# Kernel tuning notes

Hardware: AMD Instinct MI355X
Metric: run time of the kernel (lower is better)

Reference implementation:

```python
import jax, jax.numpy as jnp
import numpy as np

SEQ, BATCH, INPUT = 2048, 64, 16
HEADS, HID = 8, 64  # per-head hidden = hidden_size/output_size = 512/8


def setup_inputs() -> dict:
    key = jax.random.key(0)
    ks = jax.random.split(key, 8)
    s = 1.0 / np.sqrt(HID)  # PyTorch LSTM/Linear init scale
    return {
        "x": jax.random.normal(ks[0], (SEQ, BATCH, INPUT), jnp.float32),
        "W_ih": jax.random.uniform(ks[1], (HEADS, 4 * HID, INPUT), jnp.float32, -s, s),
        "W_hh": jax.random.uniform(ks[2], (HEADS, 4 * HID, HID), jnp.float32, -s, s),
        "b_ih": jax.random.uniform(ks[3], (HEADS, 4 * HID), jnp.float32, -s, s),
        "b_hh": jax.random.uniform(ks[4], (HEADS, 4 * HID), jnp.float32, -s, s),
        "W_lin": jax.random.uniform(ks[5], (HEADS, HID), jnp.float32, -s, s),
        "b_lin": jax.random.uniform(ks[6], (HEADS,), jnp.float32, -s, s),
    }


def _multihead_lstm(x, W_ih, W_hh, b_ih, b_hh):
    # x: (T,B,I); weights stacked over heads H. PyTorch gate order: i,f,g,o.
    T, B = x.shape[0], x.shape[1]
    H, G = W_hh.shape[0], W_hh.shape[1]  # G = 4*hid
    hid = G // 4
    # Input projection for all timesteps/heads at once: (T,B,H,4h)
    xp = jnp.einsum("tbi,hgi->tbhg", x, W_ih) + b_ih + b_hh

    def step(carry, xt):
        h_prev, c_prev = carry  # (B,H,hid)
        z = xt + jnp.einsum("bhk,hgk->bhg", h_prev, W_hh)  # (B,H,4h)
        i = jax.nn.sigmoid(z[..., 0 * hid:1 * hid])
        f = jax.nn.sigmoid(z[..., 1 * hid:2 * hid])
        g = jnp.tanh(z[..., 2 * hid:3 * hid])
        o = jax.nn.sigmoid(z[..., 3 * hid:4 * hid])
        c = f * c_prev + i * g
        h = o * jnp.tanh(c)
        return (h, c), h

    zeros = jnp.zeros((B, H, hid), x.dtype)
    _, hs = jax.lax.scan(step, (zeros, zeros), xp)  # hs: (T,B,H,hid)
    return hs


def reference(x, W_ih, W_hh, b_ih, b_hh, W_lin, b_lin):
    hs = _multihead_lstm(x, W_ih, W_hh, b_ih, b_hh)  # (T,B,H,hid)
    # per-head Linear(hid -> 1), concatenated over heads -> (T,B,H)
    out = jnp.einsum("tbhk,hk->tbh", hs, W_lin) + b_lin
    # lstm_output accumulates (sums) the per-head hidden trajectories
    lstm_output = hs.sum(axis=2)  # (T,B,hid)
    return out, lstm_output
```

## Files before the change

kernel.cpp:

```cpp
#include <hip/hip_runtime.h>
#include <hip/hip_fp16.h>

#define TT   2048
#define BB   64
#define II   16
#define HH   8
#define HIDN 64
#define GG   256
#define T4   (TT / 4)

typedef _Float16 h2 __attribute__((ext_vector_type(2)));
typedef _Float16 h4 __attribute__((ext_vector_type(4)));
typedef _Float16 h8 __attribute__((ext_vector_type(8)));

__device__ __forceinline__ float fdot2(h2 a, h2 b, float c) {
    return __builtin_amdgcn_fdot2(a, b, c, false);
}
__device__ __forceinline__ float fast_sigmoid(float z) {
    return __builtin_amdgcn_rcpf(1.0f + __expf(-z));
}
__device__ __forceinline__ float fast_tanh(float z) {
    return fmaf(2.0f, __builtin_amdgcn_rcpf(1.0f + __expf(-2.0f * z)), -1.0f);
}

__global__ void cvt_x_kernel(const float* __restrict__ x, _Float16* __restrict__ xh, int n4) {
    int i = blockIdx.x * blockDim.x + threadIdx.x;
    if (i < n4) {
        float4 v = ((const float4*)x)[i];
        ((h2*)xh)[2 * i]     = h2{ (_Float16)v.x, (_Float16)v.y };
        ((h2*)xh)[2 * i + 1] = h2{ (_Float16)v.z, (_Float16)v.w };
    }
}

template <int STAGE, bool XF16>
__global__ __launch_bounds__(64, 1)
void lstm_wave(const float* __restrict__ x,
               const _Float16* __restrict__ xh,
               const float* __restrict__ Wih,
               const float* __restrict__ Whh,
               const float* __restrict__ bih,
               const float* __restrict__ bhh,
               const float* __restrict__ Wlin,
               const float* __restrict__ blin,
               float* __restrict__ out,
               float* __restrict__ lstm_out,
               _Float16* __restrict__ stage_f16)
{
    const int lane = threadIdx.x;
    const int c    = blockIdx.x;
    const int b    = c & (BB - 1);
    const int hd   = c >> 6;

    h2 whh[4][HIDN / 2];
    h2 wih[4][II / 2];
    float bias[4];
#pragma unroll
    for (int g = 0; g < 4; ++g) {
        const int r = hd * GG + g * HIDN + lane;
        const float4* p = (const float4*)(Whh + (size_t)r * HIDN);
#pragma unroll
        for (int q = 0; q < HIDN / 4; ++q) {
            float4 v = p[q];
            whh[g][2 * q]     = h2{ (_Float16)v.x, (_Float16)v.y };
            whh[g][2 * q + 1] = h2{ (_Float16)v.z, (_Float16)v.w };
        }
        const float4* pi = (const float4*)(Wih + (size_t)r * II);
#pragma unroll
        for (int q = 0; q < II / 4; ++q) {
            float4 v = pi[q];
            wih[g][2 * q]     = h2{ (_Float16)v.x, (_Float16)v.y };
            wih[g][2 * q + 1] = h2{ (_Float16)v.z, (_Float16)v.w };
        }
        bias[g] = bih[r] + bhh[r];
    }
    float wl = 0.0f, bl = 0.0f;
    if (STAGE == 2) { wl = Wlin[hd * HIDN + lane]; bl = blin[hd]; }

    __shared__ __align__(16) _Float16 hbuf[HIDN];
    hbuf[lane] = (_Float16)0.0f;

    float cst = 0.0f;

    const _Float16* xhp = xh + b * II;
    const float*    xfp = x + b * II;
    h2 xv[II / 2];
    auto load_x = [&](int t, h2* dst) {
        int tc = t < TT ? t : TT - 1;
        if (XF16) {
            const h8* p = (const h8*)(xhp + (size_t)tc * BB * II);
            union { h8 v; h2 p2[4]; } u0, u1;
            u0.v = p[0];
            u1.v = p[1];
#pragma unroll
            for (int i = 0; i < 4; ++i) { dst[i] = u0.p2[i]; dst[4 + i] = u1.p2[i]; }
        } else {
            const float4* p = (const float4*)(xfp + (size_t)tc * BB * II);
#pragma unroll
            for (int q = 0; q < 4; ++q) {
                float4 v = p[q];
                dst[2 * q]     = h2{ (_Float16)v.x, (_Float16)v.y };
                dst[2 * q + 1] = h2{ (_Float16)v.z, (_Float16)v.w };
            }
        }
    };
    load_x(0, xv);

    h4* sptr = (h4*)(stage_f16 + (size_t)c * 256 + lane * 4);

    for (int t4 = 0; t4 < T4; ++t4) {
        union { h4 v4; h2 p2[2]; } hp;
#pragma unroll
        for (int j = 0; j < 4; ++j) {
            const int t = t4 * 4 + j;
            h2 xn[II / 2];
            load_x(t + 1, xn);

            union { h8 v[8]; h2 p[32]; } hr;
#pragma unroll
            for (int q = 0; q < 8; ++q) hr.v[q] = ((const h8*)hbuf)[q];

            float z0 = bias[0], z1 = bias[1], z2 = bias[2], z3 = bias[3];
#pragma unroll
            for (int q = 0; q < HIDN / 2; ++q) {
                z0 = fdot2(whh[0][q], hr.p[q], z0);
                z1 = fdot2(whh[1][q], hr.p[q], z1);
                z2 = fdot2(whh[2][q], hr.p[q], z2);
                z3 = fdot2(whh[3][q], hr.p[q], z3);
            }
#pragma unroll
            for (int q = 0; q < II / 2; ++q) {
                z0 = fdot2(wih[0][q], xv[q], z0);
                z1 = fdot2(wih[1][q], xv[q], z1);
                z2 = fdot2(wih[2][q], xv[q], z2);
                z3 = fdot2(wih[3][q], xv[q], z3);
            }

            float gi = fast_sigmoid(z0);
            float gf = fast_sigmoid(z1);
            float gg = fast_tanh(z2);
            float go = fast_sigmoid(z3);

            cst = fmaf(gf, cst, gi * gg);
            float h = go * fast_tanh(cst);
            _Float16 h16 = (_Float16)h;

            hbuf[lane] = h16;
            hp.p2[j >> 1][j & 1] = h16;

            if (STAGE == 2) {
                atomicAdd(&lstm_out[((size_t)t * BB + b) * HIDN + lane], h);
                float p = h * wl;
                p += __shfl_down(p, 32, 64);
                p += __shfl_down(p, 16, 64);
                p += __shfl_down(p, 8, 64);
                p += __shfl_down(p, 4, 64);
                p += __shfl_down(p, 2, 64);
                p += __shfl_down(p, 1, 64);
                if (lane == 0) out[((size_t)t * BB + b) * HH + hd] = p + bl;
            }

#pragma unroll
            for (int q = 0; q < II / 2; ++q) xv[q] = xn[q];
        }
        if (STAGE == 1) {
            *sptr = hp.v4;
            sptr += 512 * 64;
        }
    }
}

__global__ __launch_bounds__(256)
void pass_lstm(const _Float16* __restrict__ stage, float* __restrict__ lstm_out)
{
    const int tid  = threadIdx.x;
    const int k    = tid & (HIDN - 1);
    const int q    = tid >> 6;
    const int b    = blockIdx.x & (BB - 1);
    const int tile = blockIdx.x >> 6;
    const h4* sp = (const h4*)stage;

#pragma unroll
    for (int g = 0; g < 4; ++g) {
        const int t4 = tile * 16 + q + 4 * g;
        float acc0 = 0.f, acc1 = 0.f, acc2 = 0.f, acc3 = 0.f;
#pragma unroll
        for (int hd = 0; hd < HH; ++hd) {
            h4 v = sp[((size_t)t4 * 512 + hd * 64 + b) * 64 + k];
            acc0 += (float)v.x; acc1 += (float)v.y;
            acc2 += (float)v.z; acc3 += (float)v.w;
        }
        const size_t t = (size_t)t4 * 4;
        lstm_out[((t + 0) * BB + b) * HIDN + k] = acc0;
        lstm_out[((t + 1) * BB + b) * HIDN + k] = acc1;
        lstm_out[((t + 2) * BB + b) * HIDN + k] = acc2;
        lstm_out[((t + 3) * BB + b) * HIDN + k] = acc3;
    }
}

__global__ __launch_bounds__(512)
void pass_out(const _Float16* __restrict__ stage,
              const float* __restrict__ Wlin,
              const float* __restrict__ blin,
              float* __restrict__ out)
{
    __shared__ float wls[GG * 2];
    const int tid = threadIdx.x;
    wls[tid] = Wlin[tid];
    __syncthreads();

    const int b  = tid >> 3;
    const int hd = tid & 7;
    const int c  = hd * 64 + b;
    const int t4 = blockIdx.x;
    const float bl = blin[hd];

    const h4* sp = (const h4*)stage + ((size_t)t4 * 512 + c) * 64;
    float a0 = 0.f, a1 = 0.f, a2 = 0.f, a3 = 0.f;
#pragma unroll 8
    for (int k = 0; k < HIDN; ++k) {
        h4 v = sp[k];
        float w = wls[hd * HIDN + k];
        a0 = fmaf((float)v.x, w, a0);
        a1 = fmaf((float)v.y, w, a1);
        a2 = fmaf((float)v.z, w, a2);
        a3 = fmaf((float)v.w, w, a3);
    }
    const size_t t = (size_t)t4 * 4;
    out[(t + 0) * 512 + tid] = a0 + bl;
    out[(t + 1) * 512 + tid] = a1 + bl;
    out[(t + 2) * 512 + tid] = a2 + bl;
    out[(t + 3) * 512 + tid] = a3 + bl;
}

extern "C" void kernel_launch(void* const* d_in, const int* in_sizes, int n_in,
                              void* d_out, int out_size, void* d_ws, size_t ws_size,
                              hipStream_t stream)
{
    const float* x    = (const float*)d_in[0];
    const float* Wih  = (const float*)d_in[1];
    const float* Whh  = (const float*)d_in[2];
    const float* bih  = (const float*)d_in[3];
    const float* bhh  = (const float*)d_in[4];
    const float* Wlin = (const float*)d_in[5];
    const float* blin = (const float*)d_in[6];

    float* out  = (float*)d_out;
    float* lstm = out + (size_t)TT * BB * HH;

    const size_t xbytes = (size_t)TT * BB * II * 2 + 4096;
    const size_t slab16 = (size_t)TT * BB * HH * HIDN * 2;

    const bool xf16 = ws_size >= xbytes;
    _Float16* xh = (_Float16*)d_ws;
    char* slabp  = (char*)d_ws + (xf16 ? xbytes : 0);
    size_t avail = ws_size - (xf16 ? xbytes : 0);
    const int mode = (avail >= slab16) ? 1 : 2;

    if (xf16) {
        int n4 = TT * BB * II / 4;
        cvt_x_kernel<<<(n4 + 255) / 256, 256, 0, stream>>>(x, xh, n4);
    }
    if (mode == 2) {
        hipMemsetAsync(lstm, 0, (size_t)TT * BB * HIDN * 4, stream);
    }

    dim3 grid(BB * HH), block(64);
    _Float16* sh = (_Float16*)slabp;

#define LAUNCH_MAIN(M, XF) \
    lstm_wave<M, XF><<<grid, block, 0, stream>>>(x, xh, Wih, Whh, bih, bhh, Wlin, blin, out, lstm, sh)

    if (xf16) { if (mode == 1) LAUNCH_MAIN(1, true);  else LAUNCH_MAIN(2, true); }
    else      { if (mode == 1) LAUNCH_MAIN(1, false); else LAUNCH_MAIN(2, false); }
#undef LAUNCH_MAIN

    if (mode == 1) {
        pass_lstm<<<dim3(BB * 32), dim3(256), 0, stream>>>(sh, lstm);
        pass_out <<<dim3(T4), dim3(512), 0, stream>>>(sh, Wlin, blin, out);
    }
}
```

Baseline: 1.067 ms.

## Replace per-wave LSTM recurrence with MFMA-based 16-wave block kernel

```diff
diff --git a/kernel.cpp b/kernel.cpp
--- a/kernel.cpp
+++ b/kernel.cpp
@@ -12,6 +12,7 @@
 typedef _Float16 h2 __attribute__((ext_vector_type(2)));
 typedef _Float16 h4 __attribute__((ext_vector_type(4)));
 typedef _Float16 h8 __attribute__((ext_vector_type(8)));
+typedef float    f4 __attribute__((ext_vector_type(4)));
 
 __device__ __forceinline__ float fdot2(h2 a, h2 b, float c) {
     return __builtin_amdgcn_fdot2(a, b, c, false);
@@ -21,6 +22,16 @@
 }
 __device__ __forceinline__ float fast_tanh(float z) {
     return fmaf(2.0f, __builtin_amdgcn_rcpf(1.0f + __expf(-2.0f * z)), -1.0f);
+}
+
+__device__ __forceinline__ int lds_off(int b, int u) {
+    return b * 128 + ((((u >> 3) ^ b) & 7) << 4) + (u & 7) * 2;
+}
+__device__ __forceinline__ h8 cvt8(const float* p) {
+    float4 v0 = ((const float4*)p)[0];
+    float4 v1 = ((const float4*)p)[1];
+    return h8{(_Float16)v0.x, (_Float16)v0.y, (_Float16)v0.z, (_Float16)v0.w,
+              (_Float16)v1.x, (_Float16)v1.y, (_Float16)v1.z, (_Float16)v1.w};
 }
 
 __global__ void cvt_x_kernel(const float* __restrict__ x, _Float16* __restrict__ xh, int n4) {
@@ -30,6 +41,98 @@
         ((h2*)xh)[2 * i]     = h2{ (_Float16)v.x, (_Float16)v.y };
         ((h2*)xh)[2 * i + 1] = h2{ (_Float16)v.z, (_Float16)v.w };
     }
+}
+
+__global__ __launch_bounds__(1024)
+void lstm_mfma(const _Float16* __restrict__ xh,
+               const float* __restrict__ Wih,
+               const float* __restrict__ Whh,
+               const float* __restrict__ bih,
+               const float* __restrict__ bhh,
+               _Float16* __restrict__ stage_f16)
+{
+    const int tid  = threadIdx.x;
+    const int w    = tid >> 6;
+    const int lane = tid & 63;
+    const int hi   = lane >> 4;
+    const int bl   = lane & 15;
+    const int hd   = blockIdx.x >> 2;
+    const int bg   = blockIdx.x & 3;
+    const int ue   = 4 * w + hi;
+
+    const int rA = hd * GG + (bl & 3) * HIDN + 4 * w + (bl >> 2);
+    const float* pw = Whh + (size_t)rA * HIDN;
+    h8 a0 = cvt8(pw + hi * 8);
+    h8 a1 = cvt8(pw + 32 + hi * 8);
+    h8 a2{};
+    if (hi < 2) a2 = cvt8(Wih + (size_t)rA * II + hi * 8);
+
+    f4 biasv;
+#pragma unroll
+    for (int g = 0; g < 4; ++g) {
+        int r = hd * GG + g * HIDN + ue;
+        biasv[g] = bih[r] + bhh[r];
+    }
+
+    __shared__ __align__(16) char hA[2048];
+    __shared__ __align__(16) char hB[2048];
+    __shared__ __align__(16) char xA[2048];
+    __shared__ __align__(16) char xB[2048];
+
+    const int off_b0 = lds_off(bl, hi * 8);
+    const int off_b1 = lds_off(bl, 32 + hi * 8);
+    const int off_hw = lds_off(bl, ue);
+    const int off_xw = lds_off(bl, 4 * hi);
+
+    if (tid < 512) ((unsigned int*)xA)[tid] = 0u;
+    else           ((unsigned int*)xB)[tid - 512] = 0u;
+    *(_Float16*)(hA + off_hw) = (_Float16)0.0f;
+    __syncthreads();
+    const _Float16* xrow = xh + (size_t)(bg * 16 + bl) * II + 4 * hi;
+    if (w == 0) {
+        h4 xv = *(const h4*)xrow;
+        *(h4*)(xA + off_xw) = xv;
+    }
+    __syncthreads();
+
+    float cst = 0.0f;
+    h4* sptr = (h4*)stage_f16 + (size_t)(hd * 64 + bg * 16 + bl) * 64 + ue;
+
+#define STEP(jj, CURH, NXTH, CURX, NXTX) do {                                   \
+        h8 vb0 = *(const h8*)(CURH + off_b0);                                   \
+        h8 vb1 = *(const h8*)(CURH + off_b1);                                   \
+        h8 vbx = *(const h8*)(CURX + off_b0);                                   \
+        if (w == 0) {                   \
+            int tc = t0 + jj + 1; tc = tc < TT ? tc : TT - 1;                   \
+            h4 xv = *(const h4*)(xrow + (size_t)tc * (BB * II));                \
+            *(h4*)(NXTX + off_xw) = xv;                                         \
+        }                                                                       \
+        f4 acc = __builtin_amdgcn_mfma_f32_16x16x32_f16(a2, vbx, biasv, 0,0,0); \
+        acc = __builtin_amdgcn_mfma_f32_16x16x32_f16(a0, vb0, acc, 0, 0, 0);    \
+        acc = __builtin_amdgcn_mfma_f32_16x16x32_f16(a1, vb1, acc, 0, 0, 0);    \
+        float gi = fast_sigmoid(acc[0]);                                        \
+        float gf = fast_sigmoid(acc[1]);                                        \
+        float gg = fast_tanh(acc[2]);                                           \
+        float go = fast_sigmoid(acc[3]);                                        \
+        cst = fmaf(gf, cst, gi * gg);                                           \
+        float hv = go * fast_tanh(cst);                                         \
+        _Float16 h16 = (_Float16)hv;                                            \
+        *(_Float16*)(NXTH + off_hw) = h16;                                      \
+        hp.p2[jj >> 1][jj & 1] = h16;                                           \
+        __syncthreads();                                                        \
+    } while (0)
+
+    for (int t4 = 0; t4 < T4; ++t4) {
+        const int t0 = 4 * t4;
+        union { h4 v4; h2 p2[2]; } hp;
+        STEP(0, hA, hB, xA, xB);
+        STEP(1, hB, hA, xB, xA);
+        STEP(2, hA, hB, xA, xB);
+        STEP(3, hB, hA, xB, xA);
+        *sptr = hp.v4;
+        sptr += 512 * 64;
+    }
+#undef STEP
 }
 
 template <int STAGE, bool XF16>
@@ -73,8 +176,8 @@
         }
         bias[g] = bih[r] + bhh[r];
     }
-    float wl = 0.0f, bl = 0.0f;
-    if (STAGE == 2) { wl = Wlin[hd * HIDN + lane]; bl = blin[hd]; }
+    float wl = 0.0f, blv = 0.0f;
+    if (STAGE == 2) { wl = Wlin[hd * HIDN + lane]; blv = blin[hd]; }
 
     __shared__ __align__(16) _Float16 hbuf[HIDN];
     hbuf[lane] = (_Float16)0.0f;
@@ -156,7 +259,7 @@
                 p += __shfl_down(p, 4, 64);
                 p += __shfl_down(p, 2, 64);
                 p += __shfl_down(p, 1, 64);
-                if (lane == 0) out[((size_t)t * BB + b) * HH + hd] = p + bl;
+                if (lane == 0) out[((size_t)t * BB + b) * HH + hd] = p + blv;
             }
 
 #pragma unroll
@@ -260,22 +363,27 @@
         int n4 = TT * BB * II / 4;
         cvt_x_kernel<<<(n4 + 255) / 256, 256, 0, stream>>>(x, xh, n4);
     }
-    if (mode == 2) {
-        hipMemsetAsync(lstm, 0, (size_t)TT * BB * HIDN * 4, stream);
-    }
-
-    dim3 grid(BB * HH), block(64);
+
     _Float16* sh = (_Float16*)slabp;
 
-#define LAUNCH_MAIN(M, XF) \
-    lstm_wave<M, XF><<<grid, block, 0, stream>>>(x, xh, Wih, Whh, bih, bhh, Wlin, blin, out, lstm, sh)
-
-    if (xf16) { if (mode == 1) LAUNCH_MAIN(1, true);  else LAUNCH_MAIN(2, true); }
-    else      { if (mode == 1) LAUNCH_MAIN(1, false); else LAUNCH_MAIN(2, false); }
-#undef LAUNCH_MAIN
-
-    if (mode == 1) {
+    if (mode == 1 && xf16) {
+        lstm_mfma<<<dim3(HH * 4), dim3(1024), 0, stream>>>(xh, Wih, Whh, bih, bhh, sh);
         pass_lstm<<<dim3(BB * 32), dim3(256), 0, stream>>>(sh, lstm);
         pass_out <<<dim3(T4), dim3(512), 0, stream>>>(sh, Wlin, blin, out);
-    }
-}
+    } else if (mode == 1) {
+        dim3 grid(BB * HH), block(64);
+        lstm_wave<1, false><<<grid, block, 0, stream>>>(x, xh, Wih, Whh, bih, bhh,
+                                                        Wlin, blin, out, lstm, sh);
+        pass_lstm<<<dim3(BB * 32), dim3(256), 0, stream>>>(sh, lstm);
+        pass_out <<<dim3(T4), dim3(512), 0, stream>>>(sh, Wlin, blin, out);
+    } else {
+        hipMemsetAsync(lstm, 0, (size_t)TT * BB * HIDN * 4, stream);
+        dim3 grid(BB * HH), block(64);
+        if (xf16)
+            lstm_wave<2, true><<<grid, block, 0, stream>>>(x, xh, Wih, Whh, bih, bhh,
+                                                           Wlin, blin, out, lstm, sh);
+        else
+            lstm_wave<2, false><<<grid, block, 0, stream>>>(x, xh, Wih, Whh, bih, bhh,
+                                                            Wlin, blin, out, lstm, sh);
+    }
+}
```

Measured after the change: 1.158 ms. +8.6%, slower.

## Process four batch rows per wave in LSTM recurrence to reuse register weights

Applied to the files above, without the earlier changes.

```diff
diff --git a/kernel.cpp b/kernel.cpp
--- a/kernel.cpp
+++ b/kernel.cpp
@@ -29,6 +29,130 @@
         float4 v = ((const float4*)x)[i];
         ((h2*)xh)[2 * i]     = h2{ (_Float16)v.x, (_Float16)v.y };
         ((h2*)xh)[2 * i + 1] = h2{ (_Float16)v.z, (_Float16)v.w };
+    }
+}
+
+__global__ __launch_bounds__(64, 1)
+void lstm_wave4(const _Float16* __restrict__ xh,
+                const float* __restrict__ Wih,
+                const float* __restrict__ Whh,
+                const float* __restrict__ bih,
+                const float* __restrict__ bhh,
+                _Float16* __restrict__ stage_f16)
+{
+    const int lane = threadIdx.x;
+    const int hd   = blockIdx.x >> 4;
+    const int b0   = (blockIdx.x & 15) << 2;
+
+    h2 whh[4][HIDN / 2];
+    h2 wih[4][II / 2];
+    float bias[4];
+#pragma unroll
+    for (int g = 0; g < 4; ++g) {
+        const int r = hd * GG + g * HIDN + lane;
+        const float4* p = (const float4*)(Whh + (size_t)r * HIDN);
+#pragma unroll
+        for (int q = 0; q < HIDN / 4; ++q) {
+            float4 v = p[q];
+            whh[g][2 * q]     = h2{ (_Float16)v.x, (_Float16)v.y };
+            whh[g][2 * q + 1] = h2{ (_Float16)v.z, (_Float16)v.w };
+        }
+        const float4* pi = (const float4*)(Wih + (size_t)r * II);
+#pragma unroll
+        for (int q = 0; q < II / 4; ++q) {
+            float4 v = pi[q];
+            wih[g][2 * q]     = h2{ (_Float16)v.x, (_Float16)v.y };
+            wih[g][2 * q + 1] = h2{ (_Float16)v.z, (_Float16)v.w };
+        }
+        bias[g] = bih[r] + bhh[r];
+    }
+
+    __shared__ __align__(16) _Float16 hb[4][HIDN];
+#pragma unroll
+    for (int c = 0; c < 4; ++c) hb[c][lane] = (_Float16)0.0f;
+
+    float cst[4] = {0.f, 0.f, 0.f, 0.f};
+
+    const _Float16* xb0 = xh + (size_t)(b0 + 0) * II;
+    const _Float16* xb1 = xh + (size_t)(b0 + 1) * II;
+    const _Float16* xb2 = xh + (size_t)(b0 + 2) * II;
+    const _Float16* xb3 = xh + (size_t)(b0 + 3) * II;
+
+    h2 xv[4][II / 2], xn[4][II / 2];
+    auto ldx = [&](const _Float16* base, int t, h2* dst) {
+        const h8* p = (const h8*)(base + (size_t)t * (BB * II));
+        union { h8 v; h2 p2[4]; } u0, u1;
+        u0.v = p[0];
+        u1.v = p[1];
+#pragma unroll
+        for (int i = 0; i < 4; ++i) { dst[i] = u0.p2[i]; dst[4 + i] = u1.p2[i]; }
+    };
+    ldx(xb0, 0, xv[0]); ldx(xb1, 0, xv[1]); ldx(xb2, 0, xv[2]); ldx(xb3, 0, xv[3]);
+
+    h4* sp = (h4*)stage_f16 + (size_t)(hd * 64 + b0) * 64 + lane;
+
+    for (int t4 = 0; t4 < T4; ++t4) {
+        const int t0 = 4 * t4;
+        union { h4 v4; _Float16 e[4]; } hpk[4];
+#pragma unroll
+        for (int j = 0; j < 4; ++j) {
+            const int t = t0 + j;
+
+            ldx(xb0, t + 1, xn[0]); ldx(xb1, t + 1, xn[1]);
+            ldx(xb2, t + 1, xn[2]); ldx(xb3, t + 1, xn[3]);
+
+            union { h8 v[8]; h2 p[32]; } hr[4];
+#pragma unroll
+            for (int c = 0; c < 4; ++c)
+#pragma unroll
+                for (int q = 0; q < 8; ++q) hr[c].v[q] = ((const h8*)hb[c])[q];
+
+            float z[4][4];
+#pragma unroll
+            for (int c = 0; c < 4; ++c)
+#pragma unroll
+                for (int g = 0; g < 4; ++g) z[c][g] = bias[g];
+
+#pragma unroll
+            for (int q = 0; q < HIDN / 2; ++q)
+#pragma unroll
+                for (int c = 0; c < 4; ++c) {
+                    z[c][0] = fdot2(whh[0][q], hr[c].p[q], z[c][0]);
+                    z[c][1] = fdot2(whh[1][q], hr[c].p[q], z[c][1]);
+                    z[c][2] = fdot2(whh[2][q], hr[c].p[q], z[c][2]);
+                    z[c][3] = fdot2(whh[3][q], hr[c].p[q], z[c][3]);
+                }
+#pragma unroll
+            for (int q = 0; q < II / 2; ++q)
+#pragma unroll
+                for (int c = 0; c < 4; ++c) {
+                    z[c][0] = fdot2(wih[0][q], xv[c][q], z[c][0]);
+                    z[c][1] = fdot2(wih[1][q], xv[c][q], z[c][1]);
+                    z[c][2] = fdot2(wih[2][q], xv[c][q], z[c][2]);
+                    z[c][3] = fdot2(wih[3][q], xv[c][q], z[c][3]);
+                }
+
+#pragma unroll
+            for (int c = 0; c < 4; ++c) {
+                float gi = fast_sigmoid(z[c][0]);
+                float gf = fast_sigmoid(z[c][1]);
+                float gg = fast_tanh(z[c][2]);
+                float go = fast_sigmoid(z[c][3]);
+                cst[c] = fmaf(gf, cst[c], gi * gg);
+                float hv = go * fast_tanh(cst[c]);
+                _Float16 h16 = (_Float16)hv;
+                hb[c][lane] = h16;
+                hpk[c].e[j] = h16;
+            }
+#pragma unroll
+            for (int c = 0; c < 4; ++c)
+#pragma unroll
+                for (int q = 0; q < II / 2; ++q) xv[c][q] = xn[c][q];
+        }
+#pragma unroll
+        for (int c = 0; c < 4; ++c)
+            sp[c * 64] = hpk[c].v4;
+        sp += 512 * 64;
     }
 }
 
@@ -73,8 +197,8 @@
         }
         bias[g] = bih[r] + bhh[r];
     }
-    float wl = 0.0f, bl = 0.0f;
-    if (STAGE == 2) { wl = Wlin[hd * HIDN + lane]; bl = blin[hd]; }
+    float wl = 0.0f, blv = 0.0f;
+    if (STAGE == 2) { wl = Wlin[hd * HIDN + lane]; blv = blin[hd]; }
 
     __shared__ __align__(16) _Float16 hbuf[HIDN];
     hbuf[lane] = (_Float16)0.0f;
@@ -156,7 +280,7 @@
                 p += __shfl_down(p, 4, 64);
                 p += __shfl_down(p, 2, 64);
                 p += __shfl_down(p, 1, 64);
-                if (lane == 0) out[((size_t)t * BB + b) * HH + hd] = p + bl;
+                if (lane == 0) out[((size_t)t * BB + b) * HH + hd] = p + blv;
             }
 
 #pragma unroll
@@ -260,22 +384,27 @@
         int n4 = TT * BB * II / 4;
         cvt_x_kernel<<<(n4 + 255) / 256, 256, 0, stream>>>(x, xh, n4);
     }
-    if (mode == 2) {
-        hipMemsetAsync(lstm, 0, (size_t)TT * BB * HIDN * 4, stream);
-    }
-
-    dim3 grid(BB * HH), block(64);
+
     _Float16* sh = (_Float16*)slabp;
 
-#define LAUNCH_MAIN(M, XF) \
-    lstm_wave<M, XF><<<grid, block, 0, stream>>>(x, xh, Wih, Whh, bih, bhh, Wlin, blin, out, lstm, sh)
-
-    if (xf16) { if (mode == 1) LAUNCH_MAIN(1, true);  else LAUNCH_MAIN(2, true); }
-    else      { if (mode == 1) LAUNCH_MAIN(1, false); else LAUNCH_MAIN(2, false); }
-#undef LAUNCH_MAIN
-
-    if (mode == 1) {
+    if (mode == 1 && xf16) {
+        lstm_wave4<<<dim3(HH * 16), dim3(64), 0, stream>>>(xh, Wih, Whh, bih, bhh, sh);
         pass_lstm<<<dim3(BB * 32), dim3(256), 0, stream>>>(sh, lstm);
         pass_out <<<dim3(T4), dim3(512), 0, stream>>>(sh, Wlin, blin, out);
-    }
-}
+    } else if (mode == 1) {
+        dim3 grid(BB * HH), block(64);
+        lstm_wave<1, false><<<grid, block, 0, stream>>>(x, xh, Wih, Whh, bih, bhh,
+                                                        Wlin, blin, out, lstm, sh);
+        pass_lstm<<<dim3(BB * 32), dim3(256), 0, stream>>>(sh, lstm);
+        pass_out <<<dim3(T4), dim3(512), 0, stream>>>(sh, Wlin, blin, out);
+    } else {
+        hipMemsetAsync(lstm, 0, (size_t)TT * BB * HIDN * 4, stream);
+        dim3 grid(BB * HH), block(64);
+        if (xf16)
+            lstm_wave<2, true><<<grid, block, 0, stream>>>(x, xh, Wih, Whh, bih, bhh,
+                                                           Wlin, blin, out, lstm, sh);
+        else
+            lstm_wave<2, false><<<grid, block, 0, stream>>>(x, xh, Wih, Whh, bih, bhh,
+                                                            Wlin, blin, out, lstm, sh);
+    }
+}
```

Result: slower. 3.925 ms (+268.0%).
